# Kernel optimization log

Measured on AMD Instinct MI355X. Metric: run time of the kernel, lower is better.

## Reference

```python
import jax, jax.numpy as jnp
import numpy as np

N = 70000
H = 8
E = 1120000
B = 8


def setup_inputs() -> dict:
    key = jax.random.key(0)
    ks = jax.random.split(key, 12)
    inp = {
        'calcium_t': jax.random.normal(ks[0], (B, N), jnp.float32),
        'hidden': jax.random.normal(ks[1], (B, N, H), jnp.float32),
        'src': jax.random.randint(ks[2], (E,), 0, N, jnp.int32),
        'tgt': jax.random.randint(ks[3], (E,), 0, N, jnp.int32),
        'W_z_values': jax.random.normal(ks[4], (E, H), jnp.float32) * 0.01,
        'W_r_values': jax.random.normal(ks[5], (E, H), jnp.float32) * 0.01,
        'W_h_values': jax.random.normal(ks[6], (E, H), jnp.float32) * 0.01,
        'U_z': jax.random.normal(ks[7], (N, H, H), jnp.float32) * 0.01,
        'U_r': jax.random.normal(ks[8], (N, H, H), jnp.float32) * 0.01,
        'U_h': jax.random.normal(ks[9], (N, H, H), jnp.float32) * 0.01,
        'b_z': jnp.zeros((N, H), jnp.float32),
        'b_r': jnp.zeros((N, H), jnp.float32),
        'b_h': jnp.zeros((N, H), jnp.float32),
        'output_projection': jax.random.normal(ks[10], (H,), jnp.float32),
    }
    return inp


def _sparse_matmul(values, src, tgt, calcium):
    # out[b, n, h] = sum over edges e with tgt[e]==n of values[e,h]*calcium[b,src[e]]
    # (identical to coalesced COO mm: duplicate (row,col) values are summed)
    gathered = calcium.T[src]                      # (E, B)
    contrib = gathered[:, :, None] * values[:, None, :]  # (E, B, H)
    out = jax.ops.segment_sum(contrib, tgt, num_segments=N)  # (N, B, H)
    return jnp.transpose(out, (1, 0, 2))           # (B, N, H)


def reference(calcium_t, hidden, src, tgt, W_z_values, W_r_values, W_h_values,
              U_z, U_r, U_h, b_z, b_r, b_h, output_projection):
    inp_z = _sparse_matmul(W_z_values, src, tgt, calcium_t)
    inp_r = _sparse_matmul(W_r_values, src, tgt, calcium_t)
    inp_h = _sparse_matmul(W_h_values, src, tgt, calcium_t)

    rec_z = jnp.einsum('bnh,nhi->bni', hidden, U_z)
    rec_r = jnp.einsum('bnh,nhi->bni', hidden, U_r)
    z = jax.nn.sigmoid(inp_z + rec_z + b_z[None])
    r = jax.nn.sigmoid(inp_r + rec_r + b_r[None])

    rec_h = jnp.einsum('bnh,nhi->bni', r * hidden, U_h)
    h_tilde = jnp.tanh(inp_h + rec_h + b_h[None])

    hidden_new = (1.0 - z) * hidden + z * h_tilde
    calcium_t1 = jax.nn.relu(jnp.einsum('bnh,h->bn', hidden_new, output_projection))
    return calcium_t1, hidden_new
```

## Files before the change

kernel.cpp:

```cpp
#include <hip/hip_runtime.h>


__device__ __forceinline__ float fast_sigmoid(float x) {
    return 1.0f / (1.0f + __expf(-x));
}
__device__ __forceinline__ float fast_tanh(float x) {
    return 2.0f / (1.0f + __expf(-2.0f * x)) - 1.0f;
}

__device__ __forceinline__ unsigned bfr(float x) {
    unsigned u = __float_as_uint(x);
    return (u + 0x7fffu + ((u >> 16) & 1u)) >> 16;
}
__device__ __forceinline__ uint4 pack8(float4 a, float4 b) {
    uint4 r;
    r.x = bfr(a.x) | (bfr(a.y) << 16);
    r.y = bfr(a.z) | (bfr(a.w) << 16);
    r.z = bfr(b.x) | (bfr(b.y) << 16);
    r.w = bfr(b.z) | (bfr(b.w) << 16);
    return r;
}

#define BFMA(acc, p, c)                                                        \
    {                                                                          \
        acc[0] += __uint_as_float((p).x << 16) * (c);                          \
        acc[1] += __uint_as_float((p).x & 0xffff0000u) * (c);                  \
        acc[2] += __uint_as_float((p).y << 16) * (c);                          \
        acc[3] += __uint_as_float((p).y & 0xffff0000u) * (c);                  \
        acc[4] += __uint_as_float((p).z << 16) * (c);                          \
        acc[5] += __uint_as_float((p).z & 0xffff0000u) * (c);                  \
        acc[6] += __uint_as_float((p).w << 16) * (c);                          \
        acc[7] += __uint_as_float((p).w & 0xffff0000u) * (c);                  \
    }

__global__ void hist_kernel(const int* __restrict__ tgt, int* __restrict__ cnt,
                            int* __restrict__ rank, const float* __restrict__ cal,
                            float* __restrict__ calT, int N, int E) {
    int i = blockIdx.x * blockDim.x + threadIdx.x;
    if (i <= N) {
        float4* o = (float4*)(calT + (size_t)i * 8);
        if (i == N) {
            o[0] = make_float4(0.f, 0.f, 0.f, 0.f);
            o[1] = make_float4(0.f, 0.f, 0.f, 0.f);
        } else {
            float v[8];
#pragma unroll
            for (int b = 0; b < 8; ++b) v[b] = cal[(size_t)b * N + i];
            o[0] = make_float4(v[0], v[1], v[2], v[3]);
            o[1] = make_float4(v[4], v[5], v[6], v[7]);
        }
    }
    int base = i * 4;
    if (base + 3 < E) {
        int4 t = *(const int4*)(tgt + base);
        int4 r;
        r.x = atomicAdd(&cnt[t.x], 1);
        r.y = atomicAdd(&cnt[t.y], 1);
        r.z = atomicAdd(&cnt[t.z], 1);
        r.w = atomicAdd(&cnt[t.w], 1);
        *(int4*)(rank + base) = r;
    } else {
        for (int k = base; k < E; ++k) rank[k] = atomicAdd(&cnt[tgt[k]], 1);
    }
}

__global__ __launch_bounds__(256) void alloc_kernel(const int* __restrict__ cnt,
                                                    int2* __restrict__ rowCnt,
                                                    int* __restrict__ cursor, int N) {
    __shared__ int waveSum[4];
    const int n = blockIdx.x * 256 + threadIdx.x;
    const int lane = threadIdx.x & 63;
    const int wid = threadIdx.x >> 6;
    int c = (n < N) ? cnt[n] : 0;
    int pre = c;
#pragma unroll
    for (int off = 1; off < 64; off <<= 1) {
        int v = __shfl_up(pre, off, 64);
        if (lane >= off) pre += v;
    }
    if (lane == 63) waveSum[wid] = pre;
    __syncthreads();
    if (threadIdx.x == 0) {
        int s0 = waveSum[0], s1 = waveSum[1], s2 = waveSum[2], s3 = waveSum[3];
        int base = atomicAdd(cursor, s0 + s1 + s2 + s3);
        waveSum[0] = base;
        waveSum[1] = base + s0;
        waveSum[2] = base + s0 + s1;
        waveSum[3] = base + s0 + s1 + s2;
    }
    __syncthreads();
    if (n < N) rowCnt[n] = make_int2(waveSum[wid] + (pre - c), c);
}

__global__ __launch_bounds__(256) void scatter_conv(
    const int* __restrict__ src, const int* __restrict__ tgt,
    const int* __restrict__ rank, const int2* __restrict__ rowCnt,
    const float* __restrict__ Wz, const float* __restrict__ Wr,
    const float* __restrict__ Wh, const float* __restrict__ calT,
    uint4* __restrict__ recs, int E) {
    int i0 = (blockIdx.x * 256 + threadIdx.x) * 2;
    if (i0 + 1 < E) {
        int2 t2 = *(const int2*)(tgt + i0);
        int2 r2 = *(const int2*)(rank + i0);
        int2 s2 = *(const int2*)(src + i0);
        int posA = rowCnt[t2.x].x + r2.x;
        int posB = rowCnt[t2.y].x + r2.y;
        const float4* caA = (const float4*)(calT + (size_t)s2.x * 8);
        const float4* caB = (const float4*)(calT + (size_t)s2.y * 8);
        const float4* wzA = (const float4*)(Wz + (size_t)i0 * 8);
        const float4* wrA = (const float4*)(Wr + (size_t)i0 * 8);
        const float4* whA = (const float4*)(Wh + (size_t)i0 * 8);
        uint4* rpA = recs + (size_t)posA * 4;
        uint4* rpB = recs + (size_t)posB * 4;
        rpA[0] = pack8(wzA[0], wzA[1]);
        rpA[1] = pack8(wrA[0], wrA[1]);
        rpA[2] = pack8(whA[0], whA[1]);
        rpA[3] = pack8(caA[0], caA[1]);
        rpB[0] = pack8(wzA[2], wzA[3]);
        rpB[1] = pack8(wrA[2], wrA[3]);
        rpB[2] = pack8(whA[2], whA[3]);
        rpB[3] = pack8(caB[0], caB[1]);
    } else {
        for (int i = i0; i < E; ++i) {
            int pos = rowCnt[tgt[i]].x + rank[i];
            const float4* ca4 = (const float4*)(calT + (size_t)src[i] * 8);
            const float4* wz4 = (const float4*)(Wz + (size_t)i * 8);
            const float4* wr4 = (const float4*)(Wr + (size_t)i * 8);
            const float4* wh4 = (const float4*)(Wh + (size_t)i * 8);
            uint4* rp = recs + (size_t)pos * 4;
            rp[0] = pack8(wz4[0], wz4[1]);
            rp[1] = pack8(wr4[0], wr4[1]);
            rp[2] = pack8(wh4[0], wh4[1]);
            rp[3] = pack8(ca4[0], ca4[1]);
        }
    }
}

__device__ __forceinline__ float rscatter(float v[8], int lane) {
    const bool s0 = (lane & 8) != 0;
    const bool s1 = (lane & 16) != 0;
    const bool s2 = (lane & 32) != 0;
    float w0, w1, w2, w3, x0, x1;
    { float k = s0 ? v[1] : v[0], g = s0 ? v[0] : v[1]; w0 = k + __shfl_xor(g, 8, 64); }
    { float k = s0 ? v[3] : v[2], g = s0 ? v[2] : v[3]; w1 = k + __shfl_xor(g, 8, 64); }
    { float k = s0 ? v[5] : v[4], g = s0 ? v[4] : v[5]; w2 = k + __shfl_xor(g, 8, 64); }
    { float k = s0 ? v[7] : v[6], g = s0 ? v[6] : v[7]; w3 = k + __shfl_xor(g, 8, 64); }
    { float k = s1 ? w1 : w0, g = s1 ? w0 : w1; x0 = k + __shfl_xor(g, 16, 64); }
    { float k = s1 ? w3 : w2, g = s1 ? w2 : w3; x1 = k + __shfl_xor(g, 16, 64); }
    float k = s2 ? x1 : x0, g = s2 ? x0 : x1;
    return k + __shfl_xor(g, 32, 64);
}

__global__ __launch_bounds__(256) void gru_main(
    const float* __restrict__ hidden, const uint4* __restrict__ recs,
    const float* __restrict__ Uz, const float* __restrict__ Ur,
    const float* __restrict__ Uh, const float* __restrict__ bz,
    const float* __restrict__ br, const float* __restrict__ bh,
    const float* __restrict__ proj, const int2* __restrict__ rowCnt,
    float* __restrict__ outCal, float* __restrict__ outHid, int N) {
    const int lane = threadIdx.x & 63;
    const int n = blockIdx.x * 4 + (threadIdx.x >> 6);
    if (n >= N) return;
    const int s = lane >> 3;
    const int b = lane & 7;

    const int2 rc = rowCnt[n];
    const int start = rc.x;
    const int end = rc.x + rc.y;

    const float hvS = hidden[((b * N + n) << 3) + s];
    const int ub = (n << 6) + (s << 3);
    float4 uz0 = *(const float4*)(Uz + ub);
    float4 uz1 = *(const float4*)(Uz + ub + 4);
    float4 ur0 = *(const float4*)(Ur + ub);
    float4 ur1 = *(const float4*)(Ur + ub + 4);
    float4 uh0 = *(const float4*)(Uh + ub);
    float4 uh1 = *(const float4*)(Uh + ub + 4);
    const float bzS = bz[(n << 3) + s];
    const float brS = br[(n << 3) + s];
    const float bhS = bh[(n << 3) + s];
    const float pjS = proj[s];

    float az[8] = {0, 0, 0, 0, 0, 0, 0, 0};
    float ar[8] = {0, 0, 0, 0, 0, 0, 0, 0};
    float ah[8] = {0, 0, 0, 0, 0, 0, 0, 0};

    const unsigned short* recsH = (const unsigned short*)recs;
    for (int j = start + s; j < end; j += 8) {
        const uint4* rp = recs + (size_t)j * 4;
        uint4 pz = rp[0];
        uint4 pr = rp[1];
        uint4 ph = rp[2];
        unsigned cb = recsH[((size_t)j << 5) + 24 + b];
        float c = __uint_as_float(cb << 16);
        BFMA(az, pz, c);
        BFMA(ar, pr, c);
        BFMA(ah, ph, c);
    }

    az[0] += hvS * uz0.x; az[1] += hvS * uz0.y; az[2] += hvS * uz0.z; az[3] += hvS * uz0.w;
    az[4] += hvS * uz1.x; az[5] += hvS * uz1.y; az[6] += hvS * uz1.z; az[7] += hvS * uz1.w;
    ar[0] += hvS * ur0.x; ar[1] += hvS * ur0.y; ar[2] += hvS * ur0.z; ar[3] += hvS * ur0.w;
    ar[4] += hvS * ur1.x; ar[5] += hvS * ur1.y; ar[6] += hvS * ur1.z; ar[7] += hvS * ur1.w;

    float AZ = rscatter(az, lane);
    float AR = rscatter(ar, lane);
    float z = fast_sigmoid(AZ + bzS);
    float r = fast_sigmoid(AR + brS);
    float rhS = r * hvS;

    ah[0] += rhS * uh0.x; ah[1] += rhS * uh0.y; ah[2] += rhS * uh0.z; ah[3] += rhS * uh0.w;
    ah[4] += rhS * uh1.x; ah[5] += rhS * uh1.y; ah[6] += rhS * uh1.z; ah[7] += rhS * uh1.w;
    float AH = rscatter(ah, lane);
    float ht = fast_tanh(AH + bhS);
    float hn = (1.0f - z) * hvS + z * ht;

    float cv = hn * pjS;
    cv += __shfl_xor(cv, 8, 64);
    cv += __shfl_xor(cv, 16, 64);
    cv += __shfl_xor(cv, 32, 64);

    outHid[((b * N + n) << 3) + s] = hn;
    if (s == 0) outCal[b * N + n] = fmaxf(cv, 0.0f);
}

extern "C" void kernel_launch(void* const* d_in, const int* in_sizes, int n_in,
                              void* d_out, int out_size, void* d_ws, size_t ws_size,
                              hipStream_t stream) {
    const float* calcium = (const float*)d_in[0];
    const float* hidden  = (const float*)d_in[1];
    const int*   src     = (const int*)d_in[2];
    const int*   tgt     = (const int*)d_in[3];
    const float* Wz      = (const float*)d_in[4];
    const float* Wr      = (const float*)d_in[5];
    const float* Wh      = (const float*)d_in[6];
    const float* Uz      = (const float*)d_in[7];
    const float* Ur      = (const float*)d_in[8];
    const float* Uh      = (const float*)d_in[9];
    const float* bz      = (const float*)d_in[10];
    const float* br      = (const float*)d_in[11];
    const float* bh      = (const float*)d_in[12];
    const float* proj    = (const float*)d_in[13];

    const int E = in_sizes[2];
    const int H = in_sizes[13];
    const int N = in_sizes[10] / H;
    (void)n_in; (void)out_size; (void)ws_size;

    float* out = (float*)d_out;
    float* outCal = out;
    float* outHid = out + (size_t)in_sizes[0];

    char* ws = (char*)d_ws;
    int*   cnt    = (int*)ws;
    int*   cursor = (int*)(ws + (448 << 10));
    int2*  rowCnt = (int2*)(ws + (512 << 10));
    int*   rank   = (int*)(ws + (1280 << 10));
    float* calT   = (float*)(ws + (5888 << 10));
    uint4* recs   = (uint4*)(ws + (8320 << 10));

    hipMemsetAsync(ws, 0, (448 << 10) + 4, stream);

    int histThreads = (E + 3) / 4;
    hist_kernel<<<(histThreads + 255) / 256, 256, 0, stream>>>(
        tgt, cnt, rank, calcium, calT, N, E);
    alloc_kernel<<<(N + 255) / 256, 256, 0, stream>>>(cnt, rowCnt, cursor, N);
    scatter_conv<<<((E + 1) / 2 + 255) / 256, 256, 0, stream>>>(
        src, tgt, rank, rowCnt, Wz, Wr, Wh, calT, recs, E);
    gru_main<<<(N + 3) / 4, 256, 0, stream>>>(
        hidden, recs, Uz, Ur, Uh, bz, br, bh, proj,
        rowCnt, outCal, outHid, N);
}
```

Before: 192.8 us.

## Replace packed bf16 edge records with CSR edge-index gather of fp32 weights

Instead of scattering all per-edge weights and calcium into bf16 CSR-ordered records, the prep stage now writes only a CSR edge-index permutation and a per-edge gathered calcium array. The main GRU kernel then gathers the fp32 W rows by edge index. The calcium transpose moves into the allocation kernel. This drops the large packed-record write and bf16 rounding, at the cost of random 32-byte gathers of the weight arrays in the main kernel.

```diff
diff --git a/kernel.cpp b/kernel.cpp
--- a/kernel.cpp
+++ b/kernel.cpp
@@ -8,48 +8,17 @@
     return 2.0f / (1.0f + __expf(-2.0f * x)) - 1.0f;
 }
 
-__device__ __forceinline__ unsigned bfr(float x) {
-    unsigned u = __float_as_uint(x);
-    return (u + 0x7fffu + ((u >> 16) & 1u)) >> 16;
-}
-__device__ __forceinline__ uint4 pack8(float4 a, float4 b) {
-    uint4 r;
-    r.x = bfr(a.x) | (bfr(a.y) << 16);
-    r.y = bfr(a.z) | (bfr(a.w) << 16);
-    r.z = bfr(b.x) | (bfr(b.y) << 16);
-    r.w = bfr(b.z) | (bfr(b.w) << 16);
-    return r;
-}
-
-#define BFMA(acc, p, c)                                                        \
+#define FMA8F(acc, v0, v1, c)                                                  \
     {                                                                          \
-        acc[0] += __uint_as_float((p).x << 16) * (c);                          \
-        acc[1] += __uint_as_float((p).x & 0xffff0000u) * (c);                  \
-        acc[2] += __uint_as_float((p).y << 16) * (c);                          \
-        acc[3] += __uint_as_float((p).y & 0xffff0000u) * (c);                  \
-        acc[4] += __uint_as_float((p).z << 16) * (c);                          \
-        acc[5] += __uint_as_float((p).z & 0xffff0000u) * (c);                  \
-        acc[6] += __uint_as_float((p).w << 16) * (c);                          \
-        acc[7] += __uint_as_float((p).w & 0xffff0000u) * (c);                  \
+        acc[0] += (v0).x * (c); acc[1] += (v0).y * (c);                        \
+        acc[2] += (v0).z * (c); acc[3] += (v0).w * (c);                        \
+        acc[4] += (v1).x * (c); acc[5] += (v1).y * (c);                        \
+        acc[6] += (v1).z * (c); acc[7] += (v1).w * (c);                        \
     }
 
 __global__ void hist_kernel(const int* __restrict__ tgt, int* __restrict__ cnt,
-                            int* __restrict__ rank, const float* __restrict__ cal,
-                            float* __restrict__ calT, int N, int E) {
+                            int* __restrict__ rank, int E) {
     int i = blockIdx.x * blockDim.x + threadIdx.x;
-    if (i <= N) {
-        float4* o = (float4*)(calT + (size_t)i * 8);
-        if (i == N) {
-            o[0] = make_float4(0.f, 0.f, 0.f, 0.f);
-            o[1] = make_float4(0.f, 0.f, 0.f, 0.f);
-        } else {
-            float v[8];
-#pragma unroll
-            for (int b = 0; b < 8; ++b) v[b] = cal[(size_t)b * N + i];
-            o[0] = make_float4(v[0], v[1], v[2], v[3]);
-            o[1] = make_float4(v[4], v[5], v[6], v[7]);
-        }
-    }
     int base = i * 4;
     if (base + 3 < E) {
         int4 t = *(const int4*)(tgt + base);
@@ -66,7 +35,9 @@
 
 __global__ __launch_bounds__(256) void alloc_kernel(const int* __restrict__ cnt,
                                                     int2* __restrict__ rowCnt,
-                                                    int* __restrict__ cursor, int N) {
+                                                    int* __restrict__ cursor,
+                                                    const float* __restrict__ cal,
+                                                    float* __restrict__ calT, int N) {
     __shared__ int waveSum[4];
     const int n = blockIdx.x * 256 + threadIdx.x;
     const int lane = threadIdx.x & 63;
@@ -89,51 +60,31 @@
         waveSum[3] = base + s0 + s1 + s2;
     }
     __syncthreads();
-    if (n < N) rowCnt[n] = make_int2(waveSum[wid] + (pre - c), c);
-}
-
-__global__ __launch_bounds__(256) void scatter_conv(
+    if (n < N) {
+        rowCnt[n] = make_int2(waveSum[wid] + (pre - c), c);
+        float v[8];
+#pragma unroll
+        for (int b = 0; b < 8; ++b) v[b] = cal[(size_t)b * N + n];
+        float4* o = (float4*)(calT + (size_t)n * 8);
+        o[0] = make_float4(v[0], v[1], v[2], v[3]);
+        o[1] = make_float4(v[4], v[5], v[6], v[7]);
+    }
+}
+
+__global__ __launch_bounds__(256) void edge_prep(
     const int* __restrict__ src, const int* __restrict__ tgt,
     const int* __restrict__ rank, const int2* __restrict__ rowCnt,
-    const float* __restrict__ Wz, const float* __restrict__ Wr,
-    const float* __restrict__ Wh, const float* __restrict__ calT,
-    uint4* __restrict__ recs, int E) {
-    int i0 = (blockIdx.x * 256 + threadIdx.x) * 2;
-    if (i0 + 1 < E) {
-        int2 t2 = *(const int2*)(tgt + i0);
-        int2 r2 = *(const int2*)(rank + i0);
-        int2 s2 = *(const int2*)(src + i0);
-        int posA = rowCnt[t2.x].x + r2.x;
-        int posB = rowCnt[t2.y].x + r2.y;
-        const float4* caA = (const float4*)(calT + (size_t)s2.x * 8);
-        const float4* caB = (const float4*)(calT + (size_t)s2.y * 8);
-        const float4* wzA = (const float4*)(Wz + (size_t)i0 * 8);
-        const float4* wrA = (const float4*)(Wr + (size_t)i0 * 8);
-        const float4* whA = (const float4*)(Wh + (size_t)i0 * 8);
-        uint4* rpA = recs + (size_t)posA * 4;
-        uint4* rpB = recs + (size_t)posB * 4;
-        rpA[0] = pack8(wzA[0], wzA[1]);
-        rpA[1] = pack8(wrA[0], wrA[1]);
-        rpA[2] = pack8(whA[0], whA[1]);
-        rpA[3] = pack8(caA[0], caA[1]);
-        rpB[0] = pack8(wzA[2], wzA[3]);
-        rpB[1] = pack8(wrA[2], wrA[3]);
-        rpB[2] = pack8(whA[2], whA[3]);
-        rpB[3] = pack8(caB[0], caB[1]);
-    } else {
-        for (int i = i0; i < E; ++i) {
-            int pos = rowCnt[tgt[i]].x + rank[i];
-            const float4* ca4 = (const float4*)(calT + (size_t)src[i] * 8);
-            const float4* wz4 = (const float4*)(Wz + (size_t)i * 8);
-            const float4* wr4 = (const float4*)(Wr + (size_t)i * 8);
-            const float4* wh4 = (const float4*)(Wh + (size_t)i * 8);
-            uint4* rp = recs + (size_t)pos * 4;
-            rp[0] = pack8(wz4[0], wz4[1]);
-            rp[1] = pack8(wr4[0], wr4[1]);
-            rp[2] = pack8(wh4[0], wh4[1]);
-            rp[3] = pack8(ca4[0], ca4[1]);
-        }
-    }
+    const float* __restrict__ calT, int* __restrict__ eIdxCSR,
+    float* __restrict__ calE, int E) {
+    int i = blockIdx.x * 256 + threadIdx.x;
+    if (i >= E) return;
+    int t = tgt[i];
+    eIdxCSR[rowCnt[t].x + rank[i]] = i;
+    const float4* ca = (const float4*)(calT + (size_t)src[i] * 8);
+    float4 c0 = ca[0], c1 = ca[1];
+    float4* o = (float4*)(calE + (size_t)i * 8);
+    o[0] = c0;
+    o[1] = c1;
 }
 
 __device__ __forceinline__ float rscatter(float v[8], int lane) {
@@ -152,7 +103,10 @@
 }
 
 __global__ __launch_bounds__(256) void gru_main(
-    const float* __restrict__ hidden, const uint4* __restrict__ recs,
+    const float* __restrict__ hidden,
+    const int* __restrict__ eIdxCSR, const float* __restrict__ calE,
+    const float* __restrict__ Wz, const float* __restrict__ Wr,
+    const float* __restrict__ Wh,
     const float* __restrict__ Uz, const float* __restrict__ Ur,
     const float* __restrict__ Uh, const float* __restrict__ bz,
     const float* __restrict__ br, const float* __restrict__ bh,
@@ -185,17 +139,19 @@
     float ar[8] = {0, 0, 0, 0, 0, 0, 0, 0};
     float ah[8] = {0, 0, 0, 0, 0, 0, 0, 0};
 
-    const unsigned short* recsH = (const unsigned short*)recs;
     for (int j = start + s; j < end; j += 8) {
-        const uint4* rp = recs + (size_t)j * 4;
-        uint4 pz = rp[0];
-        uint4 pr = rp[1];
-        uint4 ph = rp[2];
-        unsigned cb = recsH[((size_t)j << 5) + 24 + b];
-        float c = __uint_as_float(cb << 16);
-        BFMA(az, pz, c);
-        BFMA(ar, pr, c);
-        BFMA(ah, ph, c);
+        int e = eIdxCSR[j];
+        size_t eo = (size_t)e << 3;
+        const float4* wz4 = (const float4*)(Wz + eo);
+        const float4* wr4 = (const float4*)(Wr + eo);
+        const float4* wh4 = (const float4*)(Wh + eo);
+        float4 z0 = wz4[0], z1 = wz4[1];
+        float4 r0 = wr4[0], r1 = wr4[1];
+        float4 h0 = wh4[0], h1 = wh4[1];
+        float c = calE[eo + b];
+        FMA8F(az, z0, z1, c);
+        FMA8F(ar, r0, r1, c);
+        FMA8F(ah, h0, h1, c);
     }
 
     az[0] += hvS * uz0.x; az[1] += hvS * uz0.y; az[2] += hvS * uz0.z; az[3] += hvS * uz0.w;
@@ -252,22 +208,22 @@
     float* outHid = out + (size_t)in_sizes[0];
 
     char* ws = (char*)d_ws;
-    int*   cnt    = (int*)ws;
-    int*   cursor = (int*)(ws + (448 << 10));
-    int2*  rowCnt = (int2*)(ws + (512 << 10));
-    int*   rank   = (int*)(ws + (1280 << 10));
-    float* calT   = (float*)(ws + (5888 << 10));
-    uint4* recs   = (uint4*)(ws + (8320 << 10));
+    int*   cnt     = (int*)ws;
+    int*   cursor  = (int*)(ws + (448 << 10));
+    int2*  rowCnt  = (int2*)(ws + (512 << 10));
+    int*   rank    = (int*)(ws + (1280 << 10));
+    float* calT    = (float*)(ws + (6 << 20));
+    int*   eIdxCSR = (int*)(ws + (9 << 20));
+    float* calE    = (float*)(ws + (14 << 20));
 
     hipMemsetAsync(ws, 0, (448 << 10) + 4, stream);
 
-    int histThreads = (E + 3) / 4;
-    hist_kernel<<<(histThreads + 255) / 256, 256, 0, stream>>>(
-        tgt, cnt, rank, calcium, calT, N, E);
-    alloc_kernel<<<(N + 255) / 256, 256, 0, stream>>>(cnt, rowCnt, cursor, N);
-    scatter_conv<<<((E + 1) / 2 + 255) / 256, 256, 0, stream>>>(
-        src, tgt, rank, rowCnt, Wz, Wr, Wh, calT, recs, E);
+    hist_kernel<<<((E + 3) / 4 + 255) / 256, 256, 0, stream>>>(tgt, cnt, rank, E);
+    alloc_kernel<<<(N + 255) / 256, 256, 0, stream>>>(
+        cnt, rowCnt, cursor, calcium, calT, N);
+    edge_prep<<<(E + 255) / 256, 256, 0, stream>>>(
+        src, tgt, rank, rowCnt, calT, eIdxCSR, calE, E);
     gru_main<<<(N + 3) / 4, 256, 0, stream>>>(
-        hidden, recs, Uz, Ur, Uh, bz, br, bh, proj,
+        hidden, eIdxCSR, calE, Wz, Wr, Wh, Uz, Ur, Uh, bz, br, bh, proj,
         rowCnt, outCal, outHid, N);
 }
```

After: 208.9 us. 8.4% more time.
